# Kernel tuning notes

Measured on AMD Instinct MI355X. Metric: run time of the kernel, lower is better.

## Reference

```python
import jax, jax.numpy as jnp
import numpy as np

N_NODES = 20000
N_EDGES = 320000


def gcn_conv(x, W, b, src, dst, n_nodes):
    """PyG GCNConv: add self-loops, symmetric D^-1/2 (A+I) D^-1/2 normalization,
    linear transform then normalized scatter-add aggregation, plus bias."""
    x = x @ W  # [N, out]
    loop = jnp.arange(n_nodes, dtype=src.dtype)
    s = jnp.concatenate([src, loop])  # [E+N]
    d = jnp.concatenate([dst, loop])
    # degree of destination nodes (edge weight = 1), including self-loops
    deg = jax.ops.segment_sum(jnp.ones_like(d, dtype=x.dtype), d, num_segments=n_nodes)
    dinv = jnp.where(deg > 0, jax.lax.rsqrt(deg), 0.0)
    norm = dinv[s] * dinv[d]  # [E+N]
    msg = x[s] * norm[:, None]  # gather + scale, [E+N, out]
    out = jax.ops.segment_sum(msg, d, num_segments=n_nodes)  # scatter-add
    return out + b


def setup_inputs() -> dict:
    key = jax.random.key(0)
    ks = jax.random.split(key, 8)
    x = jax.random.normal(ks[0], (N_NODES, 10), dtype=jnp.float32)
    edge_index = jax.random.randint(ks[1], (2, N_EDGES), 0, N_NODES, dtype=jnp.int32)
    # Glorot-ish init for weights, zero bias (as in PyG defaults)
    def glorot(k, shape):
        lim = float(np.sqrt(6.0 / (shape[0] + shape[1])))
        return jax.random.uniform(k, shape, jnp.float32, -lim, lim)
    return {
        "x": x,
        "edge_index": edge_index,
        "W1": glorot(ks[2], (10, 256)),
        "b1": jnp.zeros((256,), jnp.float32),
        "W2": glorot(ks[3], (256, 128)),
        "b2": jnp.zeros((128,), jnp.float32),
        "W3": glorot(ks[4], (128, 1)),
        "b3": jnp.zeros((1,), jnp.float32),
    }


def reference(x, edge_index, W1, b1, W2, b2, W3, b3):
    src, dst = edge_index[0], edge_index[1]
    n = x.shape[0]
    h = jax.nn.relu(gcn_conv(x, W1, b1, src, dst, n))
    h = jax.nn.relu(gcn_conv(h, W2, b2, src, dst, n))
    out = gcn_conv(h, W3, b3, src, dst, n)
    return out.squeeze(-1)  # [N]
```

## Files before the change

### kernel.cpp

```cpp
#include <hip/hip_runtime.h>


constexpr int NN  = 20000;
constexpr int NE  = 320000;
constexpr int F0  = 10;
constexpr int F1  = 256;
constexpr int F2  = 128;
constexpr int MB  = 16;
constexpr int CAP = 64;
constexpr int EMAX = 48;


__global__ void k_fill(const int* __restrict__ src, const int* __restrict__ dst,
                       int* cursor, int* __restrict__ col) {
  int e = blockIdx.x * 256 + threadIdx.x;
  if (e >= NE) return;
  const int d = dst[e], s = src[e];
  const int pos = atomicAdd(&cursor[d], 1) & (CAP - 1);
  col[d * CAP + pos] = s;
}


__global__ __launch_bounds__(256) void k_gemm12(
    const float* __restrict__ x, const int* __restrict__ cursor,
    const int* __restrict__ col, const float* __restrict__ W1,
    const float* __restrict__ b1, const float* __restrict__ W2,
    float* __restrict__ t2s) {
  __shared__ float alds[MB * F0];
  __shared__ float h1[MB][F1 + 4];
  __shared__ float w2lds[32 * F2];
  __shared__ int   es[MB][EMAX];
  __shared__ float ew[MB][EMAX];
  const int tid = threadIdx.x;
  const int n0 = blockIdx.x * MB;
  float4 pf0 = *((const float4*)W2 + tid);
  float4 pf1 = *((const float4*)W2 + tid + 256);
  float4 pf2 = *((const float4*)W2 + tid + 512);
  float4 pf3 = *((const float4*)W2 + tid + 768);
  {
    const int m = tid >> 4;
    const int j0 = tid & 15;
    const int n = n0 + m;
    const int deg = min(cursor[n], EMAX);
    const int base = n * CAP;
    for (int j = j0; j < deg; j += 16) {
      const int s = col[base + j];
      es[m][j] = s;
      ew[m][j] = rsqrtf((float)(cursor[s] + 1));
    }
  }
  __syncthreads();
  {
    const int m = tid >> 4;
    const int f = tid & 15;
    if (f < F0) {
      const int n = n0 + m;
      const int deg = min(cursor[n], EMAX);
      const float di = rsqrtf((float)(cursor[n] + 1));
      float acc = x[n * F0 + f] * di;
      int j = 0;
      for (; j + 3 < deg; j += 4) {
        const int s0 = es[m][j],     s1 = es[m][j + 1];
        const int s2 = es[m][j + 2], s3 = es[m][j + 3];
        const float q0 = ew[m][j],     q1 = ew[m][j + 1];
        const float q2 = ew[m][j + 2], q3 = ew[m][j + 3];
        acc += x[s0 * F0 + f] * q0 + x[s1 * F0 + f] * q1 +
               x[s2 * F0 + f] * q2 + x[s3 * F0 + f] * q3;
      }
      for (; j < deg; ++j) acc += x[es[m][j] * F0 + f] * ew[m][j];
      alds[m * F0 + f] = di * acc;
    }
  }
  __syncthreads();
  {
    const int c = tid;
    float w1r[F0];
#pragma unroll
    for (int k = 0; k < F0; ++k) w1r[k] = W1[k * F1 + c];
    const float bb = b1[c];
#pragma unroll
    for (int m = 0; m < MB; ++m) {
      float acc = bb;
#pragma unroll
      for (int k = 0; k < F0; ++k) acc += alds[m * F0 + k] * w1r[k];
      h1[m][c] = fmaxf(acc, 0.f);
    }
  }
  const int cg_ = tid & 31;
  const int m0 = (tid >> 5) * 2;
  float a00 = 0.f, a01 = 0.f, a02 = 0.f, a03 = 0.f;
  float a10 = 0.f, a11 = 0.f, a12 = 0.f, a13 = 0.f;
#define FMA4(av, bv, vw)                                            \
  a00 += (av) * (vw).x; a01 += (av) * (vw).y;                       \
  a02 += (av) * (vw).z; a03 += (av) * (vw).w;                       \
  a10 += (bv) * (vw).x; a11 += (bv) * (vw).y;                       \
  a12 += (bv) * (vw).z; a13 += (bv) * (vw).w;
  for (int kc = 0; kc < F1 / 32; ++kc) {
    __syncthreads();
    {
      float4* ldst = (float4*)w2lds;
      ldst[tid] = pf0;
      ldst[tid + 256] = pf1;
      ldst[tid + 512] = pf2;
      ldst[tid + 768] = pf3;
    }
    __syncthreads();
    if (kc + 1 < F1 / 32) {
      const float4* gnext = (const float4*)(W2 + (kc + 1) * 32 * F2);
      pf0 = gnext[tid];
      pf1 = gnext[tid + 256];
      pf2 = gnext[tid + 512];
      pf3 = gnext[tid + 768];
    }
#pragma unroll
    for (int kk = 0; kk < 32; kk += 4) {
      const int k = kc * 32 + kk;
      const float4 ha = *(const float4*)&h1[m0][k];
      const float4 hb = *(const float4*)&h1[m0 + 1][k];
      const float4 w0 = *(const float4*)&w2lds[(kk + 0) * F2 + cg_ * 4];
      const float4 w1v = *(const float4*)&w2lds[(kk + 1) * F2 + cg_ * 4];
      const float4 w2v = *(const float4*)&w2lds[(kk + 2) * F2 + cg_ * 4];
      const float4 w3v = *(const float4*)&w2lds[(kk + 3) * F2 + cg_ * 4];
      FMA4(ha.x, hb.x, w0);
      FMA4(ha.y, hb.y, w1v);
      FMA4(ha.z, hb.z, w2v);
      FMA4(ha.w, hb.w, w3v);
    }
  }
#undef FMA4
  const float d0 = rsqrtf((float)(cursor[n0 + m0] + 1));
  const float d1 = rsqrtf((float)(cursor[n0 + m0 + 1] + 1));
  *(float4*)&t2s[(size_t)(n0 + m0) * F2 + cg_ * 4] =
      make_float4(a00 * d0, a01 * d0, a02 * d0, a03 * d0);
  *(float4*)&t2s[(size_t)(n0 + m0 + 1) * F2 + cg_ * 4] =
      make_float4(a10 * d1, a11 * d1, a12 * d1, a13 * d1);
}


__global__ __launch_bounds__(256) void k_agg2(
    const float* __restrict__ t2s, const int* __restrict__ cursor,
    const int* __restrict__ col, const float* __restrict__ b2,
    const float* __restrict__ W3, float* __restrict__ t3s) {
  const int wave = (blockIdx.x * 256 + threadIdx.x) >> 6;
  const int lane = threadIdx.x & 63;
  const int half = lane >> 5;
  const int li   = lane & 31;
  const int n    = wave * 2 + half;
  if (n >= NN) return;
  const int deg = cursor[n];
  const int base = n * CAP;
  const int fx = li * 4;
  const float4 vs = *(const float4*)&t2s[(size_t)n * F2 + fx];
  float a0 = vs.x, a1 = vs.y, a2 = vs.z, a3 = vs.w;
  int k = 0;
  for (; k + 7 < deg; k += 8) {
    const int s0 = col[base + k],     s1 = col[base + k + 1];
    const int s2 = col[base + k + 2], s3 = col[base + k + 3];
    const int s4 = col[base + k + 4], s5 = col[base + k + 5];
    const int s6 = col[base + k + 6], s7 = col[base + k + 7];
    const float4 v0 = *(const float4*)&t2s[(size_t)s0 * F2 + fx];
    const float4 v1 = *(const float4*)&t2s[(size_t)s1 * F2 + fx];
    const float4 v2 = *(const float4*)&t2s[(size_t)s2 * F2 + fx];
    const float4 v3 = *(const float4*)&t2s[(size_t)s3 * F2 + fx];
    const float4 v4 = *(const float4*)&t2s[(size_t)s4 * F2 + fx];
    const float4 v5 = *(const float4*)&t2s[(size_t)s5 * F2 + fx];
    const float4 v6 = *(const float4*)&t2s[(size_t)s6 * F2 + fx];
    const float4 v7 = *(const float4*)&t2s[(size_t)s7 * F2 + fx];
    a0 += ((v0.x + v1.x) + (v2.x + v3.x)) + ((v4.x + v5.x) + (v6.x + v7.x));
    a1 += ((v0.y + v1.y) + (v2.y + v3.y)) + ((v4.y + v5.y) + (v6.y + v7.y));
    a2 += ((v0.z + v1.z) + (v2.z + v3.z)) + ((v4.z + v5.z) + (v6.z + v7.z));
    a3 += ((v0.w + v1.w) + (v2.w + v3.w)) + ((v4.w + v5.w) + (v6.w + v7.w));
  }
  for (; k + 3 < deg; k += 4) {
    const int s0 = col[base + k],     s1 = col[base + k + 1];
    const int s2 = col[base + k + 2], s3 = col[base + k + 3];
    const float4 v0 = *(const float4*)&t2s[(size_t)s0 * F2 + fx];
    const float4 v1 = *(const float4*)&t2s[(size_t)s1 * F2 + fx];
    const float4 v2 = *(const float4*)&t2s[(size_t)s2 * F2 + fx];
    const float4 v3 = *(const float4*)&t2s[(size_t)s3 * F2 + fx];
    a0 += (v0.x + v1.x) + (v2.x + v3.x);
    a1 += (v0.y + v1.y) + (v2.y + v3.y);
    a2 += (v0.z + v1.z) + (v2.z + v3.z);
    a3 += (v0.w + v1.w) + (v2.w + v3.w);
  }
  for (; k < deg; ++k) {
    const float4 v = *(const float4*)&t2s[(size_t)col[base + k] * F2 + fx];
    a0 += v.x; a1 += v.y; a2 += v.z; a3 += v.w;
  }
  const float di = rsqrtf((float)(deg + 1));
  const float4 bb = *(const float4*)&b2[fx];
  const float4 w3 = *(const float4*)&W3[fx];
  const float h0 = fmaxf(di * a0 + bb.x, 0.f);
  const float h1 = fmaxf(di * a1 + bb.y, 0.f);
  const float h2 = fmaxf(di * a2 + bb.z, 0.f);
  const float h3 = fmaxf(di * a3 + bb.w, 0.f);
  float p = (h0 * w3.x + h1 * w3.y) + (h2 * w3.z + h3 * w3.w);
#pragma unroll
  for (int off = 16; off > 0; off >>= 1) p += __shfl_down(p, off);
  if (li == 0) t3s[n] = di * p;
}


__global__ void k_agg3(const float* __restrict__ t3s, const int* __restrict__ cursor,
                       const int* __restrict__ col, const float* __restrict__ b3,
                       float* __restrict__ out) {
  int n = blockIdx.x * 256 + threadIdx.x;
  if (n >= NN) return;
  const int deg = cursor[n];
  const int base = n * CAP;
  float acc = t3s[n];
  int k = 0;
  for (; k + 7 < deg; k += 8)
    acc += ((t3s[col[base + k]] + t3s[col[base + k + 1]]) +
            (t3s[col[base + k + 2]] + t3s[col[base + k + 3]])) +
           ((t3s[col[base + k + 4]] + t3s[col[base + k + 5]]) +
            (t3s[col[base + k + 6]] + t3s[col[base + k + 7]]));
  for (; k < deg; ++k) acc += t3s[col[base + k]];
  out[n] = rsqrtf((float)(deg + 1)) * acc + b3[0];
}

extern "C" void kernel_launch(void* const* d_in, const int* in_sizes, int n_in,
                              void* d_out, int out_size, void* d_ws, size_t ws_size,
                              hipStream_t stream) {
  const float* x = (const float*)d_in[0];
  const int* ei = (const int*)d_in[1];
  const int* srcv = ei;
  const int* dstv = ei + NE;
  const float* W1 = (const float*)d_in[2];
  const float* b1 = (const float*)d_in[3];
  const float* W2 = (const float*)d_in[4];
  const float* b2 = (const float*)d_in[5];
  const float* W3 = (const float*)d_in[6];
  const float* b3 = (const float*)d_in[7];
  float* out = (float*)d_out;

  char* w = (char*)d_ws;
  auto alloc = [&](size_t bytes) -> void* {
    void* p = (void*)w;
    w += (bytes + 255) & ~(size_t)255;
    return p;
  };
  int*   cursor = (int*)  alloc(NN * 4);
  int*   col    = (int*)  alloc((size_t)NN * CAP * 4);
  float* t2s    = (float*)alloc((size_t)NN * F2 * 4);
  float* t3s    = (float*)alloc(NN * 4);

  (void)hipMemsetAsync(cursor, 0, NN * 4, stream);
  k_fill<<<(NE + 255) / 256, 256, 0, stream>>>(srcv, dstv, cursor, col);
  k_gemm12<<<NN / MB, 256, 0, stream>>>(x, cursor, col, W1, b1, W2, t2s);
  k_agg2<<<NN / 8, 256, 0, stream>>>(t2s, cursor, col, b2, W3, t3s);
  k_agg3<<<(NN + 255) / 256, 256, 0, stream>>>(t3s, cursor, col, b3, out);
}
```

Before: 147.6 us.

## Store layer-2 features in fp16 and parallelize layer-3 aggregation across lanes

```diff
diff --git a/kernel.cpp b/kernel.cpp
--- a/kernel.cpp
+++ b/kernel.cpp
@@ -1,4 +1,5 @@
 #include <hip/hip_runtime.h>
+#include <hip/hip_fp16.h>
 
 
 constexpr int NN  = 20000;
@@ -25,7 +26,7 @@
     const float* __restrict__ x, const int* __restrict__ cursor,
     const int* __restrict__ col, const float* __restrict__ W1,
     const float* __restrict__ b1, const float* __restrict__ W2,
-    float* __restrict__ t2s) {
+    __half* __restrict__ t2h) {
   __shared__ float alds[MB * F0];
   __shared__ float h1[MB][F1 + 4];
   __shared__ float w2lds[32 * F2];
@@ -130,15 +131,26 @@
 #undef FMA4
   const float d0 = rsqrtf((float)(cursor[n0 + m0] + 1));
   const float d1 = rsqrtf((float)(cursor[n0 + m0 + 1] + 1));
-  *(float4*)&t2s[(size_t)(n0 + m0) * F2 + cg_ * 4] =
-      make_float4(a00 * d0, a01 * d0, a02 * d0, a03 * d0);
-  *(float4*)&t2s[(size_t)(n0 + m0 + 1) * F2 + cg_ * 4] =
-      make_float4(a10 * d1, a11 * d1, a12 * d1, a13 * d1);
-}
-
+  union PK { uint2 u; __half2 h[2]; };
+  PK p0; p0.h[0] = __floats2half2_rn(a00 * d0, a01 * d0);
+         p0.h[1] = __floats2half2_rn(a02 * d0, a03 * d0);
+  PK p1; p1.h[0] = __floats2half2_rn(a10 * d1, a11 * d1);
+         p1.h[1] = __floats2half2_rn(a12 * d1, a13 * d1);
+  *(uint2*)&t2h[(size_t)(n0 + m0) * F2 + cg_ * 4] = p0.u;
+  *(uint2*)&t2h[(size_t)(n0 + m0 + 1) * F2 + cg_ * 4] = p1.u;
+}
+
+
+__device__ inline void acc_h4(uint2 u, float& a0, float& a1, float& a2, float& a3) {
+  union { uint2 u; __half2 h[2]; } pk;
+  pk.u = u;
+  const float2 f0 = __half22float2(pk.h[0]);
+  const float2 f1 = __half22float2(pk.h[1]);
+  a0 += f0.x; a1 += f0.y; a2 += f1.x; a3 += f1.y;
+}
 
 __global__ __launch_bounds__(256) void k_agg2(
-    const float* __restrict__ t2s, const int* __restrict__ cursor,
+    const __half* __restrict__ t2h, const int* __restrict__ cursor,
     const int* __restrict__ col, const float* __restrict__ b2,
     const float* __restrict__ W3, float* __restrict__ t3s) {
   const int wave = (blockIdx.x * 256 + threadIdx.x) >> 6;
@@ -150,42 +162,39 @@
   const int deg = cursor[n];
   const int base = n * CAP;
   const int fx = li * 4;
-  const float4 vs = *(const float4*)&t2s[(size_t)n * F2 + fx];
-  float a0 = vs.x, a1 = vs.y, a2 = vs.z, a3 = vs.w;
+  float a0 = 0.f, a1 = 0.f, a2 = 0.f, a3 = 0.f;
+  acc_h4(*(const uint2*)&t2h[(size_t)n * F2 + fx], a0, a1, a2, a3);
   int k = 0;
   for (; k + 7 < deg; k += 8) {
     const int s0 = col[base + k],     s1 = col[base + k + 1];
     const int s2 = col[base + k + 2], s3 = col[base + k + 3];
     const int s4 = col[base + k + 4], s5 = col[base + k + 5];
     const int s6 = col[base + k + 6], s7 = col[base + k + 7];
-    const float4 v0 = *(const float4*)&t2s[(size_t)s0 * F2 + fx];
-    const float4 v1 = *(const float4*)&t2s[(size_t)s1 * F2 + fx];
-    const float4 v2 = *(const float4*)&t2s[(size_t)s2 * F2 + fx];
-    const float4 v3 = *(const float4*)&t2s[(size_t)s3 * F2 + fx];
-    const float4 v4 = *(const float4*)&t2s[(size_t)s4 * F2 + fx];
-    const float4 v5 = *(const float4*)&t2s[(size_t)s5 * F2 + fx];
-    const float4 v6 = *(const float4*)&t2s[(size_t)s6 * F2 + fx];
-    const float4 v7 = *(const float4*)&t2s[(size_t)s7 * F2 + fx];
-    a0 += ((v0.x + v1.x) + (v2.x + v3.x)) + ((v4.x + v5.x) + (v6.x + v7.x));
-    a1 += ((v0.y + v1.y) + (v2.y + v3.y)) + ((v4.y + v5.y) + (v6.y + v7.y));
-    a2 += ((v0.z + v1.z) + (v2.z + v3.z)) + ((v4.z + v5.z) + (v6.z + v7.z));
-    a3 += ((v0.w + v1.w) + (v2.w + v3.w)) + ((v4.w + v5.w) + (v6.w + v7.w));
+    const uint2 v0 = *(const uint2*)&t2h[(size_t)s0 * F2 + fx];
+    const uint2 v1 = *(const uint2*)&t2h[(size_t)s1 * F2 + fx];
+    const uint2 v2 = *(const uint2*)&t2h[(size_t)s2 * F2 + fx];
+    const uint2 v3 = *(const uint2*)&t2h[(size_t)s3 * F2 + fx];
+    const uint2 v4 = *(const uint2*)&t2h[(size_t)s4 * F2 + fx];
+    const uint2 v5 = *(const uint2*)&t2h[(size_t)s5 * F2 + fx];
+    const uint2 v6 = *(const uint2*)&t2h[(size_t)s6 * F2 + fx];
+    const uint2 v7 = *(const uint2*)&t2h[(size_t)s7 * F2 + fx];
+    acc_h4(v0, a0, a1, a2, a3); acc_h4(v1, a0, a1, a2, a3);
+    acc_h4(v2, a0, a1, a2, a3); acc_h4(v3, a0, a1, a2, a3);
+    acc_h4(v4, a0, a1, a2, a3); acc_h4(v5, a0, a1, a2, a3);
+    acc_h4(v6, a0, a1, a2, a3); acc_h4(v7, a0, a1, a2, a3);
   }
   for (; k + 3 < deg; k += 4) {
     const int s0 = col[base + k],     s1 = col[base + k + 1];
     const int s2 = col[base + k + 2], s3 = col[base + k + 3];
-    const float4 v0 = *(const float4*)&t2s[(size_t)s0 * F2 + fx];
-    const float4 v1 = *(const float4*)&t2s[(size_t)s1 * F2 + fx];
-    const float4 v2 = *(const float4*)&t2s[(size_t)s2 * F2 + fx];
-    const float4 v3 = *(const float4*)&t2s[(size_t)s3 * F2 + fx];
-    a0 += (v0.x + v1.x) + (v2.x + v3.x);
-    a1 += (v0.y + v1.y) + (v2.y + v3.y);
-    a2 += (v0.z + v1.z) + (v2.z + v3.z);
-    a3 += (v0.w + v1.w) + (v2.w + v3.w);
+    const uint2 v0 = *(const uint2*)&t2h[(size_t)s0 * F2 + fx];
+    const uint2 v1 = *(const uint2*)&t2h[(size_t)s1 * F2 + fx];
+    const uint2 v2 = *(const uint2*)&t2h[(size_t)s2 * F2 + fx];
+    const uint2 v3 = *(const uint2*)&t2h[(size_t)s3 * F2 + fx];
+    acc_h4(v0, a0, a1, a2, a3); acc_h4(v1, a0, a1, a2, a3);
+    acc_h4(v2, a0, a1, a2, a3); acc_h4(v3, a0, a1, a2, a3);
   }
   for (; k < deg; ++k) {
-    const float4 v = *(const float4*)&t2s[(size_t)col[base + k] * F2 + fx];
-    a0 += v.x; a1 += v.y; a2 += v.z; a3 += v.w;
+    acc_h4(*(const uint2*)&t2h[(size_t)col[base + k] * F2 + fx], a0, a1, a2, a3);
   }
   const float di = rsqrtf((float)(deg + 1));
   const float4 bb = *(const float4*)&b2[fx];
@@ -201,22 +210,26 @@
 }
 
 
-__global__ void k_agg3(const float* __restrict__ t3s, const int* __restrict__ cursor,
-                       const int* __restrict__ col, const float* __restrict__ b3,
-                       float* __restrict__ out) {
-  int n = blockIdx.x * 256 + threadIdx.x;
+__global__ __launch_bounds__(256) void k_agg3(
+    const float* __restrict__ t3s, const int* __restrict__ cursor,
+    const int* __restrict__ col, const float* __restrict__ b3,
+    float* __restrict__ out) {
+  const int wave = (blockIdx.x * 256 + threadIdx.x) >> 6;
+  const int lane = threadIdx.x & 63;
+  const int sub  = lane >> 4;
+  const int li   = lane & 15;
+  const int n    = wave * 4 + sub;
   if (n >= NN) return;
   const int deg = cursor[n];
   const int base = n * CAP;
-  float acc = t3s[n];
-  int k = 0;
-  for (; k + 7 < deg; k += 8)
-    acc += ((t3s[col[base + k]] + t3s[col[base + k + 1]]) +
-            (t3s[col[base + k + 2]] + t3s[col[base + k + 3]])) +
-           ((t3s[col[base + k + 4]] + t3s[col[base + k + 5]]) +
-            (t3s[col[base + k + 6]] + t3s[col[base + k + 7]]));
-  for (; k < deg; ++k) acc += t3s[col[base + k]];
-  out[n] = rsqrtf((float)(deg + 1)) * acc + b3[0];
+  float acc = 0.f;
+  for (int j = li; j < deg; j += 16) acc += t3s[col[base + j]];
+  acc += __shfl_xor(acc, 8);
+  acc += __shfl_xor(acc, 4);
+  acc += __shfl_xor(acc, 2);
+  acc += __shfl_xor(acc, 1);
+  if (li == 0)
+    out[n] = rsqrtf((float)(deg + 1)) * (acc + t3s[n]) + b3[0];
 }
 
 extern "C" void kernel_launch(void* const* d_in, const int* in_sizes, int n_in,
@@ -240,14 +253,14 @@
     w += (bytes + 255) & ~(size_t)255;
     return p;
   };
-  int*   cursor = (int*)  alloc(NN * 4);
-  int*   col    = (int*)  alloc((size_t)NN * CAP * 4);
-  float* t2s    = (float*)alloc((size_t)NN * F2 * 4);
-  float* t3s    = (float*)alloc(NN * 4);
+  int*    cursor = (int*)   alloc(NN * 4);
+  int*    col    = (int*)   alloc((size_t)NN * CAP * 4);
+  __half* t2h    = (__half*)alloc((size_t)NN * F2 * 2);
+  float*  t3s    = (float*) alloc(NN * 4);
 
   (void)hipMemsetAsync(cursor, 0, NN * 4, stream);
   k_fill<<<(NE + 255) / 256, 256, 0, stream>>>(srcv, dstv, cursor, col);
-  k_gemm12<<<NN / MB, 256, 0, stream>>>(x, cursor, col, W1, b1, W2, t2s);
-  k_agg2<<<NN / 8, 256, 0, stream>>>(t2s, cursor, col, b2, W3, t3s);
-  k_agg3<<<(NN + 255) / 256, 256, 0, stream>>>(t3s, cursor, col, b3, out);
-}
+  k_gemm12<<<NN / MB, 256, 0, stream>>>(x, cursor, col, W1, b1, W2, t2h);
+  k_agg2<<<NN / 8, 256, 0, stream>>>(t2h, cursor, col, b2, W3, t3s);
+  k_agg3<<<(NN + 15) / 16, 256, 0, stream>>>(t3s, cursor, col, b3, out);
+}
```

After: 137.7 us. -6.7%, faster.
